# Performance work log

Hardware: AMD Instinct MI355X
Metric: run time of the kernel (lower is better)

Reference implementation:

```python
import jax, jax.numpy as jnp
import numpy as np

B = 65536
G = 9          # grid_size
C = 10         # num_classes
BS = 3         # block_size = sqrt(grid_size)
CONSTRAINT_WEIGHT = 0.1


def setup_inputs() -> dict:
    key = jax.random.key(0)
    k1, k2, k3 = jax.random.split(key, 3)
    logits = jax.random.normal(k1, (B, G, G, C), dtype=jnp.float32)
    targets = jax.random.randint(k2, (B, G, G), 0, C)
    puzzles = jax.random.randint(k3, (B, G, G), 0, C)
    return {"logits": logits, "targets": targets, "puzzles": puzzles}


def _sudoku_loss(logits, targets, puzzles):
    mask = (puzzles == 0).astype(logits.dtype)               # [B, G, G]

    # --- masked cross-entropy over empty cells ---
    logp = jax.nn.log_softmax(logits, axis=-1)               # [B, G, G, C]
    ce = -jnp.take_along_axis(logp, targets[..., None], axis=-1)[..., 0]
    ce_loss = (ce * mask).sum() / (mask.sum() + 1e-8)

    # --- constraint loss (rows, cols, 3x3 boxes), fully vectorized ---
    probs = jnp.exp(logp)                                    # softmax probs
    wp = probs * mask[..., None]                             # [B, G, G, C]

    def group_mse(digit_sums, msum):
        # digit_sums: [B, G_groups, C]; msum: [B, G_groups]
        # torch: per-group F.mse_loss over [B, C-1], summed over groups
        target = msum[..., None] / G                         # [B, Gg, 1]
        diff = digit_sums[..., 1:] - target                  # [B, Gg, C-1]
        return (diff * diff).mean(axis=(0, 2)).sum()

    # rows: sum over columns (axis 2)
    row_loss = group_mse(wp.sum(axis=2), mask.sum(axis=2))
    # cols: sum over rows (axis 1)
    col_loss = group_mse(wp.sum(axis=1), mask.sum(axis=1))
    # boxes: reshape to [B, bi, ri, bj, cj, C], sum within-box dims
    box_ds = wp.reshape(B, BS, BS, BS, BS, C).sum(axis=(2, 4)).reshape(B, G, C)
    box_ms = mask.reshape(B, BS, BS, BS, BS).sum(axis=(2, 4)).reshape(B, G)
    box_loss = group_mse(box_ds, box_ms)

    num_constraints = G * 2 + BS * BS                        # 27
    constraint_loss = (row_loss + col_loss + box_loss) / num_constraints

    # torch wraps the constraint loss in torch.tensor(...), detaching it
    total = ce_loss + CONSTRAINT_WEIGHT * jax.lax.stop_gradient(constraint_loss)
    return total, ce_loss, constraint_loss


def reference(logits, targets, puzzles):
    total, ce_loss, constraint_loss = _sudoku_loss(logits, targets, puzzles)
    return total, ce_loss, constraint_loss
```

## Files before the change

kernel.cpp:

```cpp
#include <hip/hip_runtime.h>


constexpr int kB = 65536;

__global__ __launch_bounds__(192) void sudoku_main(
    const float* __restrict__ logits,
    const int*   __restrict__ targets,
    const int*   __restrict__ puzzles,
    float*       __restrict__ ws)
{
    __shared__ float colacc[64 * 90];
    __shared__ float red[3][3];

    const int tid = threadIdx.x;
    for (int i = tid; i < 64 * 90; i += 192) colacc[i] = 0.f;
    __syncthreads();

    const int gt = blockIdx.x * 192 + tid;
    const int p  = gt / 3;
    const int k  = gt % 3;
    const int q  = tid / 3;

    const float* lg  = logits  + (size_t)p * 810 + (size_t)k * 270;
    const int*   tgp = targets + (size_t)p * 81  + k * 27;
    const int*   pzp = puzzles + (size_t)p * 81  + k * 27;

    int pzv[27];
    #pragma unroll
    for (int i = 0; i < 27; ++i) pzv[i] = pzp[i];

    float boxsum[3][9];
    float boxm[3] = {0.f, 0.f, 0.f};
    #pragma unroll
    for (int b = 0; b < 3; ++b)
        #pragma unroll
        for (int c = 0; c < 9; ++c) boxsum[b][c] = 0.f;

    float diff2 = 0.f, ce = 0.f, mcnt = 0.f;
    float* mycol = &colacc[q * 90];

    #pragma unroll
    for (int r = 0; r < 3; ++r) {
        float rowsum[9];
        #pragma unroll
        for (int c = 0; c < 9; ++c) rowsum[c] = 0.f;
        float rowm = 0.f;

        #pragma unroll
        for (int j = 0; j < 9; ++j) {
            const int cell = r * 9 + j;
            if (pzv[cell] == 0) {
                const float* xp = lg + cell * 10;
                float x[10];
                #pragma unroll
                for (int h = 0; h < 5; ++h) {
                    const float2 v = *(const float2*)(xp + 2 * h);
                    x[2 * h] = v.x; x[2 * h + 1] = v.y;
                }
                float mx = x[0];
                #pragma unroll
                for (int c = 1; c < 10; ++c) mx = fmaxf(mx, x[c]);
                float e[10];
                float S = 0.f;
                #pragma unroll
                for (int c = 0; c < 10; ++c) { e[c] = __expf(x[c] - mx); S += e[c]; }
                const float inv = 1.0f / S;
                const float lse = __logf(S);

                const int t = tgp[cell];
                float xt = x[0];
                #pragma unroll
                for (int c = 1; c < 10; ++c) xt = (t == c) ? x[c] : xt;
                ce   += mx + lse - xt;
                mcnt += 1.f;
                rowm += 1.f;
                const int jb = j / 3;
                boxm[jb] += 1.f;
                atomicAdd(&mycol[j * 10 + 9], 1.f);
                #pragma unroll
                for (int c = 1; c < 10; ++c) {
                    const float w = e[c] * inv;
                    rowsum[c - 1]     += w;
                    boxsum[jb][c - 1] += w;
                    atomicAdd(&mycol[j * 10 + (c - 1)], w);
                }
            }
        }
        const float tr = rowm * (1.f / 9.f);
        #pragma unroll
        for (int c = 0; c < 9; ++c) { const float d = rowsum[c] - tr; diff2 += d * d; }
    }
    #pragma unroll
    for (int b = 0; b < 3; ++b) {
        const float tb = boxm[b] * (1.f / 9.f);
        #pragma unroll
        for (int c = 0; c < 9; ++c) { const float d = boxsum[b][c] - tb; diff2 += d * d; }
    }

    __syncthreads();
    #pragma unroll
    for (int jj = 0; jj < 3; ++jj) {
        const int j = 3 * k + jj;
        const float tc = mycol[j * 10 + 9] * (1.f / 9.f);
        #pragma unroll
        for (int c = 0; c < 9; ++c) {
            const float d = mycol[j * 10 + c] - tc;
            diff2 += d * d;
        }
    }

    #pragma unroll
    for (int off = 32; off > 0; off >>= 1) {
        diff2 += __shfl_down(diff2, off);
        ce    += __shfl_down(ce, off);
        mcnt  += __shfl_down(mcnt, off);
    }
    const int wave = tid >> 6;
    if ((tid & 63) == 0) { red[0][wave] = diff2; red[1][wave] = ce; red[2][wave] = mcnt; }
    __syncthreads();
    if (tid == 0) {
        const float d  = red[0][0] + red[0][1] + red[0][2];
        const float c2 = red[1][0] + red[1][1] + red[1][2];
        const float m  = red[2][0] + red[2][1] + red[2][2];
        atomicAdd(&ws[0], d);
        atomicAdd(&ws[1], c2);
        atomicAdd(&ws[2], m);
    }
}

__global__ void sudoku_final(const float* __restrict__ ws, float* __restrict__ out)
{
    const float diff2   = ws[0];
    const float ce_sum  = ws[1];
    const float msum    = ws[2];
    const float ce_loss = ce_sum / (msum + 1e-8f);
    const float constraint = diff2 / ((float)kB * 9.f * 27.f);
    out[0] = ce_loss + 0.1f * constraint;
    out[1] = ce_loss;
    out[2] = constraint;
}

extern "C" void kernel_launch(void* const* d_in, const int* in_sizes, int n_in,
                              void* d_out, int out_size, void* d_ws, size_t ws_size,
                              hipStream_t stream)
{
    const float* logits  = (const float*)d_in[0];
    const int*   targets = (const int*)d_in[1];
    const int*   puzzles = (const int*)d_in[2];
    float* ws  = (float*)d_ws;
    float* out = (float*)d_out;

    hipMemsetAsync(d_ws, 0, 3 * sizeof(float), stream);

    const int blocks = (kB * 3) / 192;
    sudoku_main<<<blocks, 192, 0, stream>>>(logits, targets, puzzles, ws);
    sudoku_final<<<1, 1, 0, stream>>>(ws, out);
}
```

Before: 325.6 us.

## Map one thread per cell and accumulate row/col/box sums via shared atomics

Changes the work split from three threads per puzzle, each walking 27 cells serially, to one thread per cell, with 6 puzzles per 512-thread block. Row, column and box digit sums are all built with shared-memory atomics into a per-puzzle 270-float buffer, then reduced by 162 threads. This raises parallelism and makes logits loads coalesced across neighbouring cells. In exchange it adds three times as many shared atomics per cell, and 26 of the 512 threads per block sit idle.

```diff
diff --git a/kernel.cpp b/kernel.cpp
--- a/kernel.cpp
+++ b/kernel.cpp
@@ -1,112 +1,84 @@
 #include <hip/hip_runtime.h>
 
 
-constexpr int kB = 65536;
+constexpr int kB   = 65536;
+constexpr int PPB  = 6;
+constexpr int TPB  = 512;
+constexpr int CELLS = PPB * 81;
 
-__global__ __launch_bounds__(192) void sudoku_main(
+__global__ __launch_bounds__(TPB) void sudoku_main(
     const float* __restrict__ logits,
     const int*   __restrict__ targets,
     const int*   __restrict__ puzzles,
     float*       __restrict__ ws)
 {
-    __shared__ float colacc[64 * 90];
-    __shared__ float red[3][3];
+    __shared__ float acc[PPB * 270];
+    __shared__ float red[3][TPB / 64];
 
     const int tid = threadIdx.x;
-    for (int i = tid; i < 64 * 90; i += 192) colacc[i] = 0.f;
+    for (int i = tid; i < PPB * 270; i += TPB) acc[i] = 0.f;
     __syncthreads();
 
-    const int gt = blockIdx.x * 192 + tid;
-    const int p  = gt / 3;
-    const int k  = gt % 3;
-    const int q  = tid / 3;
+    const int pzbase = blockIdx.x * PPB;
+    const int q      = tid / 81;
+    const int ci     = tid - q * 81;
 
-    const float* lg  = logits  + (size_t)p * 810 + (size_t)k * 270;
-    const int*   tgp = targets + (size_t)p * 81  + k * 27;
-    const int*   pzp = puzzles + (size_t)p * 81  + k * 27;
+    float ce = 0.f, mcnt = 0.f, diff2 = 0.f;
 
-    int pzv[27];
-    #pragma unroll
-    for (int i = 0; i < 27; ++i) pzv[i] = pzp[i];
+    if (q < PPB && (pzbase + q) < kB) {
+        const int idx = pzbase * 81 + tid;
+        const int pz = puzzles[idx];
+        const int tg = targets[idx];
 
-    float boxsum[3][9];
-    float boxm[3] = {0.f, 0.f, 0.f};
-    #pragma unroll
-    for (int b = 0; b < 3; ++b)
-        #pragma unroll
-        for (int c = 0; c < 9; ++c) boxsum[b][c] = 0.f;
+        if (pz == 0) {
+            const float* xp = logits + (size_t)idx * 10;
+            float x[10];
+            #pragma unroll
+            for (int h = 0; h < 5; ++h) {
+                const float2 v = *(const float2*)(xp + 2 * h);
+                x[2 * h] = v.x; x[2 * h + 1] = v.y;
+            }
+            float mx = x[0];
+            #pragma unroll
+            for (int c = 1; c < 10; ++c) mx = fmaxf(mx, x[c]);
+            float e[10];
+            float S = 0.f;
+            #pragma unroll
+            for (int c = 0; c < 10; ++c) { e[c] = __expf(x[c] - mx); S += e[c]; }
+            const float inv = 1.0f / S;
 
-    float diff2 = 0.f, ce = 0.f, mcnt = 0.f;
-    float* mycol = &colacc[q * 90];
+            float xt = x[0];
+            #pragma unroll
+            for (int c = 1; c < 10; ++c) xt = (tg == c) ? x[c] : xt;
+            ce   = mx + __logf(S) - xt;
+            mcnt = 1.f;
 
-    #pragma unroll
-    for (int r = 0; r < 3; ++r) {
-        float rowsum[9];
-        #pragma unroll
-        for (int c = 0; c < 9; ++c) rowsum[c] = 0.f;
-        float rowm = 0.f;
-
-        #pragma unroll
-        for (int j = 0; j < 9; ++j) {
-            const int cell = r * 9 + j;
-            if (pzv[cell] == 0) {
-                const float* xp = lg + cell * 10;
-                float x[10];
-                #pragma unroll
-                for (int h = 0; h < 5; ++h) {
-                    const float2 v = *(const float2*)(xp + 2 * h);
-                    x[2 * h] = v.x; x[2 * h + 1] = v.y;
-                }
-                float mx = x[0];
-                #pragma unroll
-                for (int c = 1; c < 10; ++c) mx = fmaxf(mx, x[c]);
-                float e[10];
-                float S = 0.f;
-                #pragma unroll
-                for (int c = 0; c < 10; ++c) { e[c] = __expf(x[c] - mx); S += e[c]; }
-                const float inv = 1.0f / S;
-                const float lse = __logf(S);
-
-                const int t = tgp[cell];
-                float xt = x[0];
-                #pragma unroll
-                for (int c = 1; c < 10; ++c) xt = (t == c) ? x[c] : xt;
-                ce   += mx + lse - xt;
-                mcnt += 1.f;
-                rowm += 1.f;
-                const int jb = j / 3;
-                boxm[jb] += 1.f;
-                atomicAdd(&mycol[j * 10 + 9], 1.f);
-                #pragma unroll
-                for (int c = 1; c < 10; ++c) {
-                    const float w = e[c] * inv;
-                    rowsum[c - 1]     += w;
-                    boxsum[jb][c - 1] += w;
-                    atomicAdd(&mycol[j * 10 + (c - 1)], w);
-                }
+            const int r  = ci / 9;
+            const int j  = ci - r * 9;
+            const int bx = (r / 3) * 3 + (j / 3);
+            float* a = &acc[q * 270];
+            float* ar = a + r * 10;
+            float* ac = a + (9 + j) * 10;
+            float* ab = a + (18 + bx) * 10;
+            atomicAdd(ar + 9, 1.f);
+            atomicAdd(ac + 9, 1.f);
+            atomicAdd(ab + 9, 1.f);
+            #pragma unroll
+            for (int c = 1; c < 10; ++c) {
+                const float w = e[c] * inv;
+                atomicAdd(ar + (c - 1), w);
+                atomicAdd(ac + (c - 1), w);
+                atomicAdd(ab + (c - 1), w);
             }
         }
-        const float tr = rowm * (1.f / 9.f);
+    }
+    __syncthreads();
+
+    if (tid < PPB * 27) {
+        const float* a = &acc[tid * 10];
+        const float tm = a[9] * (1.f / 9.f);
         #pragma unroll
-        for (int c = 0; c < 9; ++c) { const float d = rowsum[c] - tr; diff2 += d * d; }
-    }
-    #pragma unroll
-    for (int b = 0; b < 3; ++b) {
-        const float tb = boxm[b] * (1.f / 9.f);
-        #pragma unroll
-        for (int c = 0; c < 9; ++c) { const float d = boxsum[b][c] - tb; diff2 += d * d; }
-    }
-
-    __syncthreads();
-    #pragma unroll
-    for (int jj = 0; jj < 3; ++jj) {
-        const int j = 3 * k + jj;
-        const float tc = mycol[j * 10 + 9] * (1.f / 9.f);
-        #pragma unroll
-        for (int c = 0; c < 9; ++c) {
-            const float d = mycol[j * 10 + c] - tc;
-            diff2 += d * d;
-        }
+        for (int c = 0; c < 9; ++c) { const float d = a[c] - tm; diff2 += d * d; }
     }
 
     #pragma unroll
@@ -119,9 +91,9 @@
     if ((tid & 63) == 0) { red[0][wave] = diff2; red[1][wave] = ce; red[2][wave] = mcnt; }
     __syncthreads();
     if (tid == 0) {
-        const float d  = red[0][0] + red[0][1] + red[0][2];
-        const float c2 = red[1][0] + red[1][1] + red[1][2];
-        const float m  = red[2][0] + red[2][1] + red[2][2];
+        float d = 0.f, c2 = 0.f, m = 0.f;
+        #pragma unroll
+        for (int w = 0; w < TPB / 64; ++w) { d += red[0][w]; c2 += red[1][w]; m += red[2][w]; }
         atomicAdd(&ws[0], d);
         atomicAdd(&ws[1], c2);
         atomicAdd(&ws[2], m);
@@ -152,7 +124,7 @@
 
     hipMemsetAsync(d_ws, 0, 3 * sizeof(float), stream);
 
-    const int blocks = (kB * 3) / 192;
-    sudoku_main<<<blocks, 192, 0, stream>>>(logits, targets, puzzles, ws);
+    const int blocks = (kB + PPB - 1) / PPB;
+    sudoku_main<<<blocks, TPB, 0, stream>>>(logits, targets, puzzles, ws);
     sudoku_final<<<1, 1, 0, stream>>>(ws, out);
 }
```

Result: slower. 669.7 us (+105.7%).
